# Kernel tuning notes

Hardware: AMD Instinct MI355X
Metric: run time of the kernel (lower is better)

The kernel has to match this reference:

```python
import jax, jax.numpy as jnp
import numpy as np

B = 8192
DIM = 1024
NI = 16
ALPHA = 0.5
BETA = 1.0


def setup_inputs() -> dict:
    key = jax.random.key(0)
    ks = jax.random.split(key, 12)
    d, n = DIM, NI
    din = d + d // n  # local expert input width = 1088
    s = 0.02  # small init scale to keep softplus in a sane range
    return {
        "y": jax.random.normal(ks[0], (B, d), jnp.float32),
        "M": jax.random.normal(ks[1], (B, d), jnp.float32),
        # global discriminator params ([in, out] layout)
        "gw0": jax.random.normal(ks[2], (d, d), jnp.float32) * s,
        "gb0": jnp.zeros((d,), jnp.float32),
        "gw1": jax.random.normal(ks[3], (d, d), jnp.float32) * s,
        "gb1": jnp.zeros((d,), jnp.float32),
        "l0w": jax.random.normal(ks[4], (2 * d, 128), jnp.float32) * s,
        "l0b": jnp.zeros((128,), jnp.float32),
        "l1w": jax.random.normal(ks[5], (128, 128), jnp.float32) * s,
        "l1b": jnp.zeros((128,), jnp.float32),
        "l2w": jax.random.normal(ks[6], (128, 1), jnp.float32) * s,
        "l2b": jnp.zeros((1,), jnp.float32),
        # local discriminator: n_interpretator stacked expert MLPs
        "lW1": jax.random.normal(ks[7], (n, din, 128), jnp.float32) * s,
        "lb1": jnp.zeros((n, 128), jnp.float32),
        "lW2": jax.random.normal(ks[8], (n, 128, 128), jnp.float32) * s,
        "lb2": jnp.zeros((n, 128), jnp.float32),
        "lW3": jax.random.normal(ks[9], (n, 128, 1), jnp.float32) * s,
        "lb3": jnp.zeros((n, 1), jnp.float32),
        "n_interpretator": NI,
    }


def reference(y, M, gw0, gb0, gw1, gb1, l0w, l0b, l1w, l1b, l2w, l2b,
              lW1, lb1, lW2, lb2, lW3, lb3, n_interpretator):
    n = n_interpretator
    Bsz, d = y.shape
    M3 = M.reshape(Bsz, d // n, n)                              # [B, d/n, n]
    Mp3 = jnp.concatenate([M3[1:], M3[:1]], axis=0)             # shuffled negatives
    y_exp = jnp.broadcast_to(y[:, :, None], (Bsz, d, n))        # [B, d, n]
    yM = jnp.concatenate([M3, y_exp], axis=1)                   # [B, d/n + d, n]
    yMp = jnp.concatenate([Mp3, y_exp], axis=1)

    def local_d(x):
        # batched over the n expert groups: grouped GEMMs instead of a loop
        h = jax.nn.relu(jnp.einsum('bdn,ndh->bnh', x, lW1) + lb1)   # [B, n, 128]
        h = jax.nn.relu(jnp.einsum('bnh,nhk->bnk', h, lW2) + lb2)   # [B, n, 128]
        s = jnp.einsum('bnh,nho->bno', h, lW3) + lb3                # [B, n, 1]
        return s[..., 0]                                            # [B, n]

    Ej_l = -jnp.mean(jax.nn.softplus(-local_d(yM)))
    Em_l = jnp.mean(jax.nn.softplus(local_d(yMp)))
    LOCAL = (Em_l - Ej_l) * BETA

    def global_d(yy, Mm):
        h = jax.nn.relu(Mm.reshape(Bsz, -1) @ gw0 + gb0) @ gw1 + gb1  # net(M)
        h = jnp.concatenate([yy, h], axis=1)                          # [B, 2d]
        h = jax.nn.relu(h @ l0w + l0b)
        h = jax.nn.relu(h @ l1w + l1b)
        return h @ l2w + l2b                                          # [B, 1]

    Ej_g = -jnp.mean(jax.nn.softplus(-global_d(y, M3)))
    Em_g = jnp.mean(jax.nn.softplus(global_d(y, Mp3)))
    GLOBAL = (Em_g - Ej_g) * ALPHA

    return LOCAL + GLOBAL
```

## Files before the change

kernel.cpp:

```cpp
#include <hip/hip_runtime.h>
#include <hip/hip_bf16.h>
#include <math.h>

#define B_ROWS 8192
#define NEXP 16

typedef __attribute__((ext_vector_type(8))) short short8;
typedef __attribute__((ext_vector_type(4))) float f32x4;

__device__ __forceinline__ float softplus_f(float x) {
    return fmaxf(x, 0.f) + log1pf(expf(-fabsf(x)));
}

__device__ __forceinline__ float bf2f(short u) {
    union { unsigned int i; float f; } c;
    c.i = ((unsigned int)(unsigned short)u) << 16;
    return c.f;
}

__device__ __forceinline__ short f2bf_s(float x) {
    __hip_bfloat16 h = __float2bfloat16(x);
    return *(short*)&h;
}

__device__ __forceinline__ void gll16(const void* g, void* l) {
    __builtin_amdgcn_global_load_lds(
        (const __attribute__((address_space(1))) void*)g,
        (__attribute__((address_space(3))) void*)l, 16, 0, 0);
}

#define FENCE() asm volatile("" ::: "memory")
#define VM3 asm volatile("s_waitcnt vmcnt(3)" ::: "memory")
#define VM0 asm volatile("s_waitcnt vmcnt(0)" ::: "memory")
#define BAR __builtin_amdgcn_s_barrier()

__device__ void cast_body(const float* in, __hip_bfloat16* out, int blk, int tid) {
    int i = blk * 256 + tid;
    float4 v = ((const float4*)in)[i];
    union { ushort4 u; __hip_bfloat16 h[4]; } p;
    p.h[0] = __float2bfloat16(v.x);
    p.h[1] = __float2bfloat16(v.y);
    p.h[2] = __float2bfloat16(v.z);
    p.h[3] = __float2bfloat16(v.w);
    ((ushort4*)out)[i] = p.u;
}

__global__ __launch_bounds__(256) void prep_all(
    const float* __restrict__ y, const float* __restrict__ M,
    const float* __restrict__ lW1, const float* __restrict__ gw0,
    const float* __restrict__ l0w, const float* __restrict__ gb1,
    const float* __restrict__ l0b, const float* __restrict__ lW2,
    const float* __restrict__ l1w, const float* __restrict__ gw1,
    __hip_bfloat16* __restrict__ yb, short* __restrict__ Mt2,
    __hip_bfloat16* __restrict__ W1yt, short* __restrict__ W1m2,
    __hip_bfloat16* __restrict__ W0p, __hip_bfloat16* __restrict__ l0wyt,
    float* __restrict__ bing, short* __restrict__ W2sb,
    short* __restrict__ L1ws, __hip_bfloat16* __restrict__ WgTb,
    double* __restrict__ acc, int* __restrict__ counter)
{
    __shared__ __align__(16) char smem[66048];
    const int b = blockIdx.x;
    const int tid = threadIdx.x;
    const int lane = tid & 63, w = tid >> 6;

    if (b < 8) {
        short* As = (short*)smem;
        short* Bs = (short*)(smem + 16384);
        const int bn = b * 128;
        const int wr = w >> 1, wc = w & 1;
        const int l15 = lane & 15, l4 = lane >> 4;

        f32x4 acc4[4][4] = {};
        for (int k0 = 0; k0 < 1024; k0 += 64) {
            {
                int c4 = (tid & 31) * 4;
                int kkr0 = tid >> 5;
                #pragma unroll
                for (int r = 0; r < 8; ++r) {
                    int kk = r * 8 + kkr0;
                    float4 v = *(const float4*)&l0w[(long)(1024 + k0 + kk) * 128 + c4];
                    int g = kk >> 3, sub = kk & 7;
                    #pragma unroll
                    for (int i = 0; i < 4; ++i) {
                        int row = c4 + i;
                        As[row * 64 + (g ^ (row & 7)) * 8 + sub] = f2bf_s(((const float*)&v)[i]);
                    }
                }
            }
            {
                int jr0 = tid >> 3;
                int g = tid & 7;
                #pragma unroll
                for (int s = 0; s < 4; ++s) {
                    int jrel = s * 32 + jr0;
                    const float* src = &gw1[(long)(bn + jrel) * 1024 + k0 + g * 8];
                    float4 v0 = *(const float4*)src;
                    float4 v1 = *(const float4*)(src + 4);
                    union { short8 v; short sh[8]; } o;
                    o.sh[0] = f2bf_s(v0.x); o.sh[1] = f2bf_s(v0.y);
                    o.sh[2] = f2bf_s(v0.z); o.sh[3] = f2bf_s(v0.w);
                    o.sh[4] = f2bf_s(v1.x); o.sh[5] = f2bf_s(v1.y);
                    o.sh[6] = f2bf_s(v1.z); o.sh[7] = f2bf_s(v1.w);
                    *(short8*)&Bs[jrel * 64 + (g ^ (jrel & 7)) * 8] = o.v;
                }
            }
            __syncthreads();
            #pragma unroll
            for (int st = 0; st < 2; ++st) {
                const int gr = (st * 4 + l4) ^ (l15 & 7);
                short8 a[4], bv[4];
                #pragma unroll
                for (int m = 0; m < 4; ++m)
                    a[m] = *(const short8*)&As[(wr * 64 + m * 16 + l15) * 64 + gr * 8];
                #pragma unroll
                for (int n = 0; n < 4; ++n)
                    bv[n] = *(const short8*)&Bs[(wc * 64 + n * 16 + l15) * 64 + gr * 8];
                #pragma unroll
                for (int m = 0; m < 4; ++m)
                    #pragma unroll
                    for (int n = 0; n < 4; ++n)
                        acc4[m][n] = __builtin_amdgcn_mfma_f32_16x16x32_bf16(a[m], bv[n], acc4[m][n], 0, 0, 0);
            }
            __syncthreads();
        }
        #pragma unroll
        for (int m = 0; m < 4; ++m) {
            int row = wr * 64 + m * 16 + l4 * 4;
            #pragma unroll
            for (int n = 0; n < 4; ++n) {
                int col = bn + wc * 64 + n * 16 + l15;
                #pragma unroll
                for (int r = 0; r < 4; ++r)
                    WgTb[(long)(row + r) * 1024 + col] = __float2bfloat16(acc4[m][n][r]);
            }
        }
        return;
    }

    if (b < 8200) { cast_body(y, yb, b - 8, tid); return; }

    if (b < 9224) {
        short* t = (short*)smem;
        const long r0 = (long)(b - 8200) * 8;
        #pragma unroll
        for (int i = 0; i < 8; ++i) {
            int idx = i * 1024 + tid * 4;
            float4 v = *(const float4*)&M[r0 * 1024 + idx];
            short4 s;
            s.x = f2bf_s(v.x); s.y = f2bf_s(v.y); s.z = f2bf_s(v.z); s.w = f2bf_s(v.w);
            *(short4*)&t[idx] = s;
        }
        __syncthreads();
        const int e = tid & 15, rr = (tid >> 4) & 7, hf = tid >> 7;
        #pragma unroll
        for (int c = 0; c < 4; ++c) {
            union { short8 v; short s[8]; } o;
            #pragma unroll
            for (int j = 0; j < 8; ++j)
                o.s[j] = t[rr * 1024 + (hf * 32 + c * 8 + j) * 16 + e];
            *(short8*)&Mt2[(long)(e >> 1) * (8192L * 128) + (r0 + rr) * 128
                           + (e & 1) * 64 + hf * 32 + c * 8] = o.v;
        }
        return;
    }

    float (*t)[129] = (float(*)[129])smem;

    if (b < 9736) {
        int l = b - 9224, bx = l & 15, by = l >> 4;
        int n0 = bx * 128, k0 = by * 32;
        long base = 64L * 128 + (long)bx * (1088L * 128);
        #pragma unroll
        for (int ll = 0; ll < 16; ++ll) {
            int idx = tid + ll * 256;
            int kk = idx >> 7, nn = idx & 127;
            t[kk][nn] = lW1[base + (long)(k0 + kk) * 128 + nn];
        }
        __syncthreads();
        int nn = tid >> 1, kb = (tid & 1) * 16;
        #pragma unroll
        for (int j = 0; j < 16; ++j)
            W1yt[(long)(n0 + nn) * 1024 + k0 + kb + j] = __float2bfloat16(t[kb + j][nn]);
        return;
    }

    if (b < 9768) {
        int l = b - 9736, bx = l & 15, by = l >> 4;
        int n0 = bx * 128, k0 = by * 32;
        long base = (long)bx * (1088L * 128);
        #pragma unroll
        for (int ll = 0; ll < 16; ++ll) {
            int idx = tid + ll * 256;
            int kk = idx >> 7, nn = idx & 127;
            if (kk < 32) t[kk][nn] = lW1[base + (long)(k0 + kk) * 128 + nn];
        }
        __syncthreads();
        int nn = tid >> 1, kb = (tid & 1) * 16;
        int half = bx & 1;
        #pragma unroll
        for (int j = 0; j < 16; ++j) {
            W1m2[(long)(n0 + nn) * 128 + half * 64 + k0 + kb + j] = f2bf_s(t[kb + j][nn]);
            W1m2[(long)(n0 + nn) * 128 + (1 - half) * 64 + k0 + kb + j] = 0;
        }
        return;
    }

    if (b < 10024) {
        int l = b - 9768, bx = l & 7, by = l >> 3;
        int n0 = bx * 128, k0 = by * 32;
        int e = k0 >> 6, dd0 = k0 & 63;
        #pragma unroll
        for (int ll = 0; ll < 16; ++ll) {
            int idx = tid + ll * 256;
            int kk = idx >> 7, nn = idx & 127;
            t[kk][nn] = gw0[(long)((dd0 + kk) * 16 + e) * 1024 + n0 + nn];
        }
        __syncthreads();
        int nn = tid >> 1, kb = (tid & 1) * 16;
        #pragma unroll
        for (int j = 0; j < 16; ++j)
            W0p[(long)(n0 + nn) * 1024 + k0 + kb + j] = __float2bfloat16(t[kb + j][nn]);
        return;
    }

    if (b < 10056) {
        int by = b - 10024;
        int k0 = by * 32;
        #pragma unroll
        for (int ll = 0; ll < 16; ++ll) {
            int idx = tid + ll * 256;
            int kk = idx >> 7, nn = idx & 127;
            t[kk][nn] = l0w[(long)(k0 + kk) * 128 + nn];
        }
        __syncthreads();
        int nn = tid >> 1, kb = (tid & 1) * 16;
        #pragma unroll
        for (int j = 0; j < 16; ++j)
            l0wyt[(long)nn * 1024 + k0 + kb + j] = __float2bfloat16(t[kb + j][nn]);
        return;
    }

    if (b == 10056) {
        if (tid < 128) {
            float s = l0b[tid];
            for (int o = 0; o < 1024; ++o)
                s = fmaf(gb1[o], l0w[(1024 + o) * 128 + tid], s);
            bing[tid] = s;
        }
        if (tid == 255) { acc[0] = 0.0; acc[1] = 0.0; *counter = 0; }
        return;
    }

    {
        int bb = b - 10057;
        const float* in = (bb < 16) ? lW2 + (long)bb * 16384 : l1w;
        short* out = (bb < 16) ? W2sb + (long)bb * 16384 : L1ws;
        #pragma unroll
        for (int l = 0; l < 64; ++l) {
            int idx = l * 256 + tid;
            t[idx >> 7][idx & 127] = in[idx];
        }
        __syncthreads();
        #pragma unroll
        for (int l = 0; l < 8; ++l) {
            int c = l * 256 + tid;
            int col = c >> 4, kc = c & 15;
            int kcs = kc ^ (col & 7);
            union { short8 v; short s[8]; } u;
            #pragma unroll
            for (int j = 0; j < 8; ++j)
                u.s[j] = f2bf_s(t[kc * 8 + j][col]);
            *(short8*)&out[col * 128 + kcs * 8] = u.v;
        }
    }
}

__global__ __launch_bounds__(512, 4) void gemm3s(
    const short* __restrict__ yb, const short* __restrict__ W1yt,
    __hip_bfloat16* __restrict__ Y1b,
    const short* __restrict__ Mt2, const short* __restrict__ W1m2,
    __hip_bfloat16* __restrict__ Mpb,
    const short* __restrict__ W0p, const float* __restrict__ gb0,
    __hip_bfloat16* __restrict__ H0b)
{
    __shared__ __align__(16) char smem[73728];
    const int tid = threadIdx.x;
    const int lane = tid & 63, w = tid >> 6;
    const int l15 = lane & 15, l4 = lane >> 4;
    const int wr = w >> 2, wc = w & 3;

    const int bid = blockIdx.x;
    const int xcd = bid & 7;
    const int idx = bid >> 3;

    int grp, bm, bn, K;
    const short* A; const short* Wt; __hip_bfloat16* C; int ldc;
    if (idx < 64) {
        grp = 0; const int c = idx >> 3, r = idx & 7;
        bm = (xcd * 8 + r) * 128; bn = c * 256;
        A = yb; Wt = W1yt + (long)bn * 1024; K = 1024; C = Y1b; ldc = 2048;
    } else if (idx < 96) {
        int j = idx - 64; const int c = j >> 3, r = j & 7;
        grp = 2; bm = (xcd * 8 + r) * 128; bn = c * 256;
        A = Mt2; Wt = W0p + (long)bn * 1024; K = 1024; C = H0b; ldc = 1024;
    } else {
        int j = idx - 96; const int c = j >> 3, r = j & 7;
        grp = 1; bm = (xcd * 8 + r) * 128; bn = c * 256;
        A = Mt2 + (long)c * (8192L * 128);
        Wt = W1m2 + (long)bn * 128; K = 128; C = Mpb; ldc = 2048;
    }
    const int nt = K >> 5;

    const int rowA = tid >> 2;
    const int sgA  = (tid & 3) ^ ((rowA >> 1) & 3);
    const int rowB0 = tid >> 2;
    const int sgB0  = (tid & 3) ^ ((rowB0 >> 1) & 3);
    const int rowB1 = (tid + 512) >> 2;
    const int sgB1  = (tid & 3) ^ ((rowB1 >> 1) & 3);

    auto STAGE = [&](int t, int sl) {
        char* base = smem + sl * 24576;
        const short* asrc;
        if (grp == 2) {
            const int g = t * 4 + sgA;
            asrc = A + (long)(g >> 4) * (8192L * 128)
                     + (long)(bm + rowA) * 128 + (g & 15) * 8;
        } else {
            asrc = A + (long)(bm + rowA) * K + t * 32 + sgA * 8;
        }
        gll16(asrc, base + w * 1024);
        gll16(Wt + (long)rowB0 * K + t * 32 + sgB0 * 8,
              base + 8192 + w * 1024);
        gll16(Wt + (long)rowB1 * K + t * 32 + sgB1 * 8,
              base + 16384 + w * 1024);
    };

    f32x4 acc[4][4] = {};
    const int xr = (l4 ^ ((l15 >> 1) & 3)) * 16;
    const int aOff = (wr * 64 + l15) * 64 + xr;
    const int bOff = 8192 + (wc * 64 + l15) * 64 + xr;

    auto PHASE = [&](int sl, int tn, int sl2, int mode) {
        const char* base = smem + sl * 24576;
        short8 a_[4], b_[4];
        #pragma unroll
        for (int m = 0; m < 4; ++m)
            a_[m] = *(const short8*)(base + aOff + m * 1024);
        #pragma unroll
        for (int n = 0; n < 4; ++n)
            b_[n] = *(const short8*)(base + bOff + n * 1024);
        if (mode == 0) { STAGE(tn, sl2); VM3; }
        else if (mode == 1) { VM0; }
        FENCE(); BAR; FENCE();
        __builtin_amdgcn_s_setprio(1);
        #pragma unroll
        for (int m = 0; m < 4; ++m)
            #pragma unroll
            for (int n = 0; n < 4; ++n)
                acc[m][n] = __builtin_amdgcn_mfma_f32_16x16x32_bf16(
                    a_[m], b_[n], acc[m][n], 0, 0, 0);
        __builtin_amdgcn_s_setprio(0);
        FENCE(); BAR; FENCE();
    };

    STAGE(0, 0);
    STAGE(1, 1);
    VM3; FENCE(); BAR; FENCE();

    int sl = 0, sl2 = 2;
    for (int t = 0; t < nt - 2; ++t) {
        PHASE(sl, t + 2, sl2, 0);
        sl = (sl == 2) ? 0 : sl + 1;
        sl2 = (sl2 == 2) ? 0 : sl2 + 1;
    }
    PHASE(sl, 0, 0, 1);
    sl = (sl == 2) ? 0 : sl + 1;
    PHASE(sl, 0, 0, 2);

    #pragma unroll
    for (int m = 0; m < 4; ++m) {
        const int row = bm + wr * 64 + m * 16 + l4 * 4;
        #pragma unroll
        for (int n = 0; n < 4; ++n) {
            const int col = bn + wc * 64 + n * 16 + l15;
            const float bv = (grp == 2) ? gb0[col] : 0.f;
            #pragma unroll
            for (int r = 0; r < 4; ++r) {
                float v = acc[m][n][r] + bv;
                if (grp == 2) v = fmaxf(v, 0.f);
                C[(long)(row + r) * ldc + col] = __float2bfloat16(v);
            }
        }
    }
}

__global__ __launch_bounds__(256) void tail_plus(
    const __hip_bfloat16* __restrict__ Yp, const __hip_bfloat16* __restrict__ Mq,
    const float* __restrict__ bin, const short* __restrict__ W2s,
    const float* __restrict__ b2, const float* __restrict__ w3,
    const float* __restrict__ b3, double* __restrict__ acc,
    const short* __restrict__ H0b, const short* __restrict__ WgTb,
    __hip_bfloat16* __restrict__ Tgb,
    const short* __restrict__ ybs, const short* __restrict__ l0ws,
    __hip_bfloat16* __restrict__ Tyb)
{
    __shared__ __align__(16) char smem[68096];
    const int bid = blockIdx.x;
    const int tid = threadIdx.x;
    const int lane = tid & 63;
    const int l15 = lane & 15, l4 = lane >> 4;

    if (bid >= 2048) {
        const int sel = bid - 2048;
        const short* Ain = (sel < 64) ? H0b : ybs;
        const short* Bin = (sel < 64) ? WgTb : l0ws;
        __hip_bfloat16* Co = (sel < 64) ? Tgb : Tyb;
        short* As = (short*)smem;
        short* Bs = (short*)(smem + 16384);
        const int w = tid >> 6;
        const int wr = w >> 1, wc = w & 1;
        const int bm = (sel & 63) * 128;
        const int srow = lane >> 3;
        const int gsrc = (lane & 7) ^ srow;

        f32x4 a4[4][4] = {};
        for (int k0 = 0; k0 < 1024; k0 += 64) {
            #pragma unroll
            for (int s = 0; s < 4; ++s) {
                const int rrel = s * 32 + w * 8 + srow;
                gll16(Ain + (long)(bm + rrel) * 1024 + k0 + gsrc * 8,
                      As + (s * 32 + w * 8) * 64);
                gll16(Bin + (long)rrel * 1024 + k0 + gsrc * 8,
                      Bs + (s * 32 + w * 8) * 64);
            }
            __syncthreads();
            #pragma unroll
            for (int st = 0; st < 2; ++st) {
                const int gr = (st * 4 + l4) ^ (l15 & 7);
                short8 a[4], b[4];
                #pragma unroll
                for (int m = 0; m < 4; ++m)
                    a[m] = *(const short8*)&As[(wr * 64 + m * 16 + l15) * 64 + gr * 8];
                #pragma unroll
                for (int n = 0; n < 4; ++n)
                    b[n] = *(const short8*)&Bs[(wc * 64 + n * 16 + l15) * 64 + gr * 8];
                #pragma unroll
                for (int m = 0; m < 4; ++m)
                    #pragma unroll
                    for (int n = 0; n < 4; ++n)
                        a4[m][n] = __builtin_amdgcn_mfma_f32_16x16x32_bf16(a[m], b[n], a4[m][n], 0, 0, 0);
            }
            __syncthreads();
        }
        #pragma unroll
        for (int m = 0; m < 4; ++m) {
            int row = bm + (w >> 1) * 64 + m * 16 + l4 * 4;
            #pragma unroll
            for (int n = 0; n < 4; ++n) {
                int col = (w & 1) * 64 + n * 16 + l15;
                #pragma unroll
                for (int r = 0; r < 4; ++r)
                    Co[(long)(row + r) * 128 + col] = __float2bfloat16(a4[m][n][r]);
            }
        }
        return;
    }

    const int wkid = (bid & 7) * 256 + (bid >> 3);
    const int e = wkid & 15;
    const int b0 = (wkid >> 4) * 64;
    const int cbase = e * 128;
    const int wid = tid >> 6;
    const int side = wid >> 1;
    const int wr = wid & 1;
    const int widthIn = 2048;

    short* h1 = (short*)smem;
    short* Bs = (short*)(smem + 32768);
    float* bins = (float*)(smem + 65536);
    float* b2s  = (float*)(smem + 66048);
    float* w3s  = (float*)(smem + 66560);
    float* red  = (float*)(smem + 67072);

    const short* W2e = W2s + (long)e * 16384;
    #pragma unroll
    for (int l = 0; l < 8; ++l) {
        int cb = (l * 4 + wid) * 64;
        gll16(W2e + (long)(cb + lane) * 8, &Bs[cb * 8]);
    }
    if (tid < 128) {
        bins[tid] = bin[cbase + tid];
        b2s[tid]  = b2[cbase + tid];
        w3s[tid]  = w3[cbase + tid];
    }
    __syncthreads();

    const short* Ys = (const short*)Yp;
    const short* Ms = (const short*)Mq;
    #pragma unroll
    for (int c = 0; c < 4; ++c) {
        int chunk = c * 256 + tid;
        int row = chunk >> 4, kc = chunk & 15;
        short8 yv = *(const short8*)&Ys[(long)(b0 + row) * widthIn + cbase + kc * 8];
        float yf[8];
        #pragma unroll
        for (int j = 0; j < 8; ++j) yf[j] = bf2f(yv[j]) + bins[kc * 8 + j];
        int dst = row * 128 + (kc ^ (row & 7)) * 8;
        #pragma unroll
        for (int s = 0; s < 2; ++s) {
            int rowm = (b0 + row + s) & (B_ROWS - 1);
            short8 mv = *(const short8*)&Ms[(long)rowm * widthIn + cbase + kc * 8];
            union { short8 v; short sh[8]; } o;
            #pragma unroll
            for (int j = 0; j < 8; ++j)
                o.sh[j] = f2bf_s(fmaxf(yf[j] + bf2f(mv[j]), 0.f));
            *(short8*)&h1[s * 8192 + dst] = o.v;
        }
    }
    __syncthreads();

    f32x4 accv[2][8] = {};
    #pragma unroll
    for (int st = 0; st < 4; ++st) {
        short8 a[2], b[8];
        #pragma unroll
        for (int m = 0; m < 2; ++m) {
            int row = wr * 32 + m * 16 + l15;
            int ch = (st * 4 + l4) ^ (row & 7);
            a[m] = *(const short8*)&h1[side * 8192 + row * 128 + ch * 8];
        }
        #pragma unroll
        for (int n = 0; n < 8; ++n) {
            int col = n * 16 + l15;
            int ch = (st * 4 + l4) ^ (col & 7);
            b[n] = *(const short8*)&Bs[col * 128 + ch * 8];
        }
        #pragma unroll
        for (int m = 0; m < 2; ++m)
            #pragma unroll
            for (int n = 0; n < 8; ++n)
                accv[m][n] = __builtin_amdgcn_mfma_f32_16x16x32_bf16(a[m], b[n], accv[m][n], 0, 0, 0);
    }

    float p[2][4] = {};
    #pragma unroll
    for (int m = 0; m < 2; ++m)
        #pragma unroll
        for (int n = 0; n < 8; ++n) {
            int colL = n * 16 + l15;
            float bb = b2s[colL], ww = w3s[colL];
            #pragma unroll
            for (int r = 0; r < 4; ++r) {
                float h2 = fmaxf(accv[m][n][r] + bb, 0.f);
                p[m][r] = fmaf(h2, ww, p[m][r]);
            }
        }
    #pragma unroll
    for (int m = 0; m < 2; ++m)
        #pragma unroll
        for (int r = 0; r < 4; ++r)
            #pragma unroll
            for (int off = 1; off < 16; off <<= 1)
                p[m][r] += __shfl_xor(p[m][r], off, 64);

    float mysum = 0.f;
    if (l15 == 0) {
        float bb = b3[e];
        #pragma unroll
        for (int m = 0; m < 2; ++m)
            #pragma unroll
            for (int r = 0; r < 4; ++r) {
                float s = p[m][r] + bb;
                mysum += softplus_f(side ? s : -s);
            }
    }
    red[tid] = mysum;
    __syncthreads();
    for (int s2 = 128; s2 > 0; s2 >>= 1) {
        if (tid < s2) red[tid] += red[tid + s2];
        __syncthreads();
    }
    if (tid == 0) atomicAdd(acc, (double)red[0]);
}

__global__ __launch_bounds__(256) void tail_mfma(
    const __hip_bfloat16* __restrict__ Yp, const __hip_bfloat16* __restrict__ Mq,
    const float* __restrict__ bin,
    const short* __restrict__ W2s,
    const float* __restrict__ b2, const float* __restrict__ w3,
    const float* __restrict__ b3,
    int widthIn, double* __restrict__ acc, int* __restrict__ counter,
    float* __restrict__ out)
{
    const int b0 = blockIdx.x * 64;
    const int e = blockIdx.y;
    const int cbase = e * 128;
    const int tid = threadIdx.x;
    const int lane = tid & 63;
    const int wid = tid >> 6;
    const int side = wid >> 1;
    const int wr = wid & 1;

    __shared__ __align__(16) short h1[2 * 64 * 128];
    __shared__ __align__(16) short Bs[128 * 128];
    __shared__ float bins[128], b2s[128], w3s[128];
    __shared__ float red[256];

    const short* W2e = W2s + (long)e * 16384;
    #pragma unroll
    for (int l = 0; l < 8; ++l) {
        int cb = (l * 4 + wid) * 64;
        gll16(W2e + (long)(cb + lane) * 8, &Bs[cb * 8]);
    }
    if (tid < 128) {
        bins[tid] = bin[cbase + tid];
        b2s[tid]  = b2[cbase + tid];
        w3s[tid]  = w3[cbase + tid];
    }
    __syncthreads();

    const short* Ys = (const short*)Yp;
    const short* Ms = (const short*)Mq;
    #pragma unroll
    for (int c = 0; c < 4; ++c) {
        int chunk = c * 256 + tid;
        int row = chunk >> 4, kc = chunk & 15;
        short8 yv = *(const short8*)&Ys[(long)(b0 + row) * widthIn + cbase + kc * 8];
        float yf[8];
        #pragma unroll
        for (int j = 0; j < 8; ++j) yf[j] = bf2f(yv[j]) + bins[kc * 8 + j];
        int dst = row * 128 + (kc ^ (row & 7)) * 8;
        #pragma unroll
        for (int s = 0; s < 2; ++s) {
            int rowm = (b0 + row + s) & (B_ROWS - 1);
            short8 mv = *(const short8*)&Ms[(long)rowm * widthIn + cbase + kc * 8];
            union { short8 v; short sh[8]; } o;
            #pragma unroll
            for (int j = 0; j < 8; ++j)
                o.sh[j] = f2bf_s(fmaxf(yf[j] + bf2f(mv[j]), 0.f));
            *(short8*)&h1[s * 8192 + dst] = o.v;
        }
    }
    __syncthreads();

    const int l15 = lane & 15, l4 = lane >> 4;
    f32x4 accv[2][8] = {};
    #pragma unroll
    for (int st = 0; st < 4; ++st) {
        short8 a[2], b[8];
        #pragma unroll
        for (int m = 0; m < 2; ++m) {
            int row = wr * 32 + m * 16 + l15;
            int ch = (st * 4 + l4) ^ (row & 7);
            a[m] = *(const short8*)&h1[side * 8192 + row * 128 + ch * 8];
        }
        #pragma unroll
        for (int n = 0; n < 8; ++n) {
            int col = n * 16 + l15;
            int ch = (st * 4 + l4) ^ (col & 7);
            b[n] = *(const short8*)&Bs[col * 128 + ch * 8];
        }
        #pragma unroll
        for (int m = 0; m < 2; ++m)
            #pragma unroll
            for (int n = 0; n < 8; ++n)
                accv[m][n] = __builtin_amdgcn_mfma_f32_16x16x32_bf16(a[m], b[n], accv[m][n], 0, 0, 0);
    }

    float p[2][4] = {};
    #pragma unroll
    for (int m = 0; m < 2; ++m)
        #pragma unroll
        for (int n = 0; n < 8; ++n) {
            int colL = n * 16 + l15;
            float bb = b2s[colL], ww = w3s[colL];
            #pragma unroll
            for (int r = 0; r < 4; ++r) {
                float h2 = fmaxf(accv[m][n][r] + bb, 0.f);
                p[m][r] = fmaf(h2, ww, p[m][r]);
            }
        }
    #pragma unroll
    for (int m = 0; m < 2; ++m)
        #pragma unroll
        for (int r = 0; r < 4; ++r)
            #pragma unroll
            for (int off = 1; off < 16; off <<= 1)
                p[m][r] += __shfl_xor(p[m][r], off, 64);

    float mysum = 0.f;
    if (l15 == 0) {
        float bb = b3[e];
        #pragma unroll
        for (int m = 0; m < 2; ++m)
            #pragma unroll
            for (int r = 0; r < 4; ++r) {
                float s = p[m][r] + bb;
                mysum += softplus_f(side ? s : -s);
            }
    }
    red[tid] = mysum;
    __syncthreads();
    for (int s2 = 128; s2 > 0; s2 >>= 1) {
        if (tid < s2) red[tid] += red[tid + s2];
        __syncthreads();
    }
    if (tid == 0) {
        atomicAdd(acc + 1, (double)red[0]);
        __threadfence();
        int old = atomicAdd(counter, 1);
        if (old == (int)(gridDim.x * gridDim.y) - 1) {
            double a0 = atomicAdd(acc + 0, 0.0);
            double a1 = atomicAdd(acc + 1, 0.0);
            out[0] = (float)(a0 / (8192.0 * 16.0) + 0.5 * a1 / 8192.0);
        }
    }
}

extern "C" void kernel_launch(void* const* d_in, const int* in_sizes, int n_in,
                              void* d_out, int out_size, void* d_ws, size_t ws_size,
                              hipStream_t stream)
{
    const float* y   = (const float*)d_in[0];
    const float* M   = (const float*)d_in[1];
    const float* gw0 = (const float*)d_in[2];
    const float* gb0 = (const float*)d_in[3];
    const float* gw1 = (const float*)d_in[4];
    const float* gb1 = (const float*)d_in[5];
    const float* l0w = (const float*)d_in[6];
    const float* l0b = (const float*)d_in[7];
    const float* l1w = (const float*)d_in[8];
    const float* l1b = (const float*)d_in[9];
    const float* l2w = (const float*)d_in[10];
    const float* l2b = (const float*)d_in[11];
    const float* lW1 = (const float*)d_in[12];
    const float* lb1 = (const float*)d_in[13];
    const float* lW2 = (const float*)d_in[14];
    const float* lb2 = (const float*)d_in[15];
    const float* lW3 = (const float*)d_in[16];
    const float* lb3 = (const float*)d_in[17];

    char* w = (char*)d_ws;
    double* acc = (double*)w;
    int* counter = (int*)(w + 16);
    float* bing = (float*)(w + 256);
    const size_t MB = 1u << 20;
    __hip_bfloat16* Y1b  = (__hip_bfloat16*)(w + 4096);
    __hip_bfloat16* Mpb  = (__hip_bfloat16*)(w + 4096 + 32 * MB);
    __hip_bfloat16* H0b  = (__hip_bfloat16*)(w + 4096 + 64 * MB);
    short*          Mt2  = (short*)(w + 4096 + 80 * MB);
    __hip_bfloat16* yb   = (__hip_bfloat16*)(w + 4096 + 96 * MB);
    __hip_bfloat16* W1yt = (__hip_bfloat16*)(w + 4096 + 112 * MB);
    __hip_bfloat16* W0p  = (__hip_bfloat16*)(w + 4096 + 118 * MB);
    __hip_bfloat16* l0wyt = (__hip_bfloat16*)(w + 4096 + 120 * MB);
    short* W2sb = (short*)(w + 4096 + 120 * MB + 512 * 1024);
    short* L1ws = (short*)(w + 4096 + 121 * MB);
    __hip_bfloat16* WgTb = (__hip_bfloat16*)(w + 4096 + 121 * MB + 512 * 1024);
    short* W1m2 = (short*)(w + 4096 + 122 * MB);
    __hip_bfloat16* Tyb = (__hip_bfloat16*)(w + 4096 + 123 * MB);
    __hip_bfloat16* Tgb = (__hip_bfloat16*)(w + 4096 + 125 * MB);

    dim3 blk(256);

    prep_all<<<dim3(10074), blk, 0, stream>>>(
        y, M, lW1, gw0, l0w, gb1, l0b, lW2, l1w, gw1,
        yb, Mt2, W1yt, W1m2, W0p, l0wyt, bing, W2sb, L1ws, WgTb,
        acc, counter);

    gemm3s<<<dim3(1280), dim3(512), 0, stream>>>(
        (const short*)yb, (const short*)W1yt, Y1b,
        Mt2, W1m2, Mpb,
        (const short*)W0p, gb0, H0b);

    tail_plus<<<dim3(2176), blk, 0, stream>>>(
        Y1b, Mpb, lb1, W2sb, lb2, lW3, lb3, acc,
        (const short*)H0b, (const short*)WgTb, Tgb,
        (const short*)yb, (const short*)l0wyt, Tyb);

    tail_mfma<<<dim3(128, 1), blk, 0, stream>>>(
        Tyb, Tgb, bing, L1ws, l1b, l2w, l2b, 128, acc, counter,
        (float*)d_out);
}
```

Baseline: 196.6 us.

## Split-K the weight-fold GEMM in prep and reduce partials inside gemm3s

The small weight-product GEMM in prep_all (8 blocks looping over all of K) becomes 64 blocks, each handling a 128-wide K slice and writing fp32 partials. Eight extra blocks appended to gemm3s sum the partials and cast them to bf16 WgTb. The y cast now does 8 float4 per thread over 1024 blocks instead of one per block, and the lW2/l1w transpose is done in two halves so shared memory halves. The aim is to stop the long serial GEMM blocks from becoming the tail of prep_all and to cut block count and LDS use. The cost is extra partial traffic, and the wgtp buffer aliases Tyb/Tgb, which are written only later in tail_plus.

```diff
diff --git a/kernel.cpp b/kernel.cpp
--- a/kernel.cpp
+++ b/kernel.cpp
@@ -33,17 +33,6 @@
 #define VM3 asm volatile("s_waitcnt vmcnt(3)" ::: "memory")
 #define VM0 asm volatile("s_waitcnt vmcnt(0)" ::: "memory")
 #define BAR __builtin_amdgcn_s_barrier()
-
-__device__ void cast_body(const float* in, __hip_bfloat16* out, int blk, int tid) {
-    int i = blk * 256 + tid;
-    float4 v = ((const float4*)in)[i];
-    union { ushort4 u; __hip_bfloat16 h[4]; } p;
-    p.h[0] = __float2bfloat16(v.x);
-    p.h[1] = __float2bfloat16(v.y);
-    p.h[2] = __float2bfloat16(v.z);
-    p.h[3] = __float2bfloat16(v.w);
-    ((ushort4*)out)[i] = p.u;
-}
 
 __global__ __launch_bounds__(256) void prep_all(
     const float* __restrict__ y, const float* __restrict__ M,
@@ -55,23 +44,25 @@
     __hip_bfloat16* __restrict__ W1yt, short* __restrict__ W1m2,
     __hip_bfloat16* __restrict__ W0p, __hip_bfloat16* __restrict__ l0wyt,
     float* __restrict__ bing, short* __restrict__ W2sb,
-    short* __restrict__ L1ws, __hip_bfloat16* __restrict__ WgTb,
+    short* __restrict__ L1ws, float* __restrict__ wgtp,
     double* __restrict__ acc, int* __restrict__ counter)
 {
-    __shared__ __align__(16) char smem[66048];
+    __shared__ __align__(16) char smem[33280];
     const int b = blockIdx.x;
     const int tid = threadIdx.x;
     const int lane = tid & 63, w = tid >> 6;
 
-    if (b < 8) {
+    if (b < 64) {
         short* As = (short*)smem;
         short* Bs = (short*)(smem + 16384);
-        const int bn = b * 128;
+        const int ct = b & 7, ks = b >> 3;
+        const int bn = ct * 128;
         const int wr = w >> 1, wc = w & 1;
         const int l15 = lane & 15, l4 = lane >> 4;
 
         f32x4 acc4[4][4] = {};
-        for (int k0 = 0; k0 < 1024; k0 += 64) {
+        for (int kq = 0; kq < 2; ++kq) {
+            const int k0 = ks * 128 + kq * 64;
             {
                 int c4 = (tid & 31) * 4;
                 int kkr0 = tid >> 5;
@@ -131,17 +122,31 @@
                 int col = bn + wc * 64 + n * 16 + l15;
                 #pragma unroll
                 for (int r = 0; r < 4; ++r)
-                    WgTb[(long)(row + r) * 1024 + col] = __float2bfloat16(acc4[m][n][r]);
-            }
-        }
-        return;
-    }
-
-    if (b < 8200) { cast_body(y, yb, b - 8, tid); return; }
-
-    if (b < 9224) {
+                    wgtp[((long)ks * 128 + row + r) * 1024 + col] = acc4[m][n][r];
+            }
+        }
+        return;
+    }
+
+    if (b < 1088) {
+        const long base = (long)(b - 64) * 2048;
+        #pragma unroll
+        for (int j = 0; j < 8; ++j) {
+            long i = base + j * 256 + tid;
+            float4 v = ((const float4*)y)[i];
+            union { ushort4 u; __hip_bfloat16 h[4]; } p;
+            p.h[0] = __float2bfloat16(v.x);
+            p.h[1] = __float2bfloat16(v.y);
+            p.h[2] = __float2bfloat16(v.z);
+            p.h[3] = __float2bfloat16(v.w);
+            ((ushort4*)yb)[i] = p.u;
+        }
+        return;
+    }
+
+    if (b < 2112) {
         short* t = (short*)smem;
-        const long r0 = (long)(b - 8200) * 8;
+        const long r0 = (long)(b - 1088) * 8;
         #pragma unroll
         for (int i = 0; i < 8; ++i) {
             int idx = i * 1024 + tid * 4;
@@ -166,8 +171,8 @@
 
     float (*t)[129] = (float(*)[129])smem;
 
-    if (b < 9736) {
-        int l = b - 9224, bx = l & 15, by = l >> 4;
+    if (b < 2624) {
+        int l = b - 2112, bx = l & 15, by = l >> 4;
         int n0 = bx * 128, k0 = by * 32;
         long base = 64L * 128 + (long)bx * (1088L * 128);
         #pragma unroll
@@ -184,8 +189,8 @@
         return;
     }
 
-    if (b < 9768) {
-        int l = b - 9736, bx = l & 15, by = l >> 4;
+    if (b < 2656) {
+        int l = b - 2624, bx = l & 15, by = l >> 4;
         int n0 = bx * 128, k0 = by * 32;
         long base = (long)bx * (1088L * 128);
         #pragma unroll
@@ -205,8 +210,8 @@
         return;
     }
 
-    if (b < 10024) {
-        int l = b - 9768, bx = l & 7, by = l >> 3;
+    if (b < 2912) {
+        int l = b - 2656, bx = l & 7, by = l >> 3;
         int n0 = bx * 128, k0 = by * 32;
         int e = k0 >> 6, dd0 = k0 & 63;
         #pragma unroll
@@ -223,8 +228,8 @@
         return;
     }
 
-    if (b < 10056) {
-        int by = b - 10024;
+    if (b < 2944) {
+        int by = b - 2912;
         int k0 = by * 32;
         #pragma unroll
         for (int ll = 0; ll < 16; ++ll) {
@@ -240,7 +245,7 @@
         return;
     }
 
-    if (b == 10056) {
+    if (b == 2944) {
         if (tid < 128) {
             float s = l0b[tid];
             for (int o = 0; o < 1024; ++o)
@@ -252,25 +257,31 @@
     }
 
     {
-        int bb = b - 10057;
+        int bb = b - 2945;
         const float* in = (bb < 16) ? lW2 + (long)bb * 16384 : l1w;
         short* out = (bb < 16) ? W2sb + (long)bb * 16384 : L1ws;
-        #pragma unroll
-        for (int l = 0; l < 64; ++l) {
-            int idx = l * 256 + tid;
-            t[idx >> 7][idx & 127] = in[idx];
-        }
-        __syncthreads();
-        #pragma unroll
-        for (int l = 0; l < 8; ++l) {
-            int c = l * 256 + tid;
-            int col = c >> 4, kc = c & 15;
-            int kcs = kc ^ (col & 7);
-            union { short8 v; short s[8]; } u;
-            #pragma unroll
-            for (int j = 0; j < 8; ++j)
-                u.s[j] = f2bf_s(t[kc * 8 + j][col]);
-            *(short8*)&out[col * 128 + kcs * 8] = u.v;
+        float (*t2)[65] = (float(*)[65])smem;
+        #pragma unroll
+        for (int h = 0; h < 2; ++h) {
+            if (h) __syncthreads();
+            #pragma unroll
+            for (int l = 0; l < 32; ++l) {
+                int idx = l * 256 + tid;
+                int kk = idx >> 6, cc = idx & 63;
+                t2[kk][cc] = in[(long)kk * 128 + h * 64 + cc];
+            }
+            __syncthreads();
+            #pragma unroll
+            for (int l = 0; l < 4; ++l) {
+                int c2 = l * 256 + tid;
+                int col = h * 64 + (c2 >> 4), kc = c2 & 15;
+                int kcs = kc ^ (col & 7);
+                union { short8 v; short s[8]; } u;
+                #pragma unroll
+                for (int j = 0; j < 8; ++j)
+                    u.s[j] = f2bf_s(t2[kc * 8 + j][col - h * 64]);
+                *(short8*)&out[col * 128 + kcs * 8] = u.v;
+            }
         }
     }
 }
@@ -281,7 +292,8 @@
     const short* __restrict__ Mt2, const short* __restrict__ W1m2,
     __hip_bfloat16* __restrict__ Mpb,
     const short* __restrict__ W0p, const float* __restrict__ gb0,
-    __hip_bfloat16* __restrict__ H0b)
+    __hip_bfloat16* __restrict__ H0b,
+    const float* __restrict__ wgtp, __hip_bfloat16* __restrict__ WgTb)
 {
     __shared__ __align__(16) char smem[73728];
     const int tid = threadIdx.x;
@@ -290,6 +302,31 @@
     const int wr = w >> 2, wc = w & 3;
 
     const int bid = blockIdx.x;
+
+    if (bid >= 1280) {
+        const int rb = bid - 1280;
+        #pragma unroll
+        for (int j = 0; j < 8; ++j) {
+            int i4 = tid + j * 512;
+            int flat = i4 * 4;
+            int row = flat >> 7, cc = flat & 127;
+            const long base = (long)row * 1024 + rb * 128 + cc;
+            f32x4 s = {};
+            #pragma unroll
+            for (int ks = 0; ks < 8; ++ks) {
+                f32x4 v = *(const f32x4*)&wgtp[(long)ks * 131072 + base];
+                s += v;
+            }
+            union { ushort4 u; __hip_bfloat16 h[4]; } o;
+            o.h[0] = __float2bfloat16(s[0]);
+            o.h[1] = __float2bfloat16(s[1]);
+            o.h[2] = __float2bfloat16(s[2]);
+            o.h[3] = __float2bfloat16(s[3]);
+            *(ushort4*)&WgTb[base] = o.u;
+        }
+        return;
+    }
+
     const int xcd = bid & 7;
     const int idx = bid >> 3;
 
@@ -759,18 +796,20 @@
     short* W1m2 = (short*)(w + 4096 + 122 * MB);
     __hip_bfloat16* Tyb = (__hip_bfloat16*)(w + 4096 + 123 * MB);
     __hip_bfloat16* Tgb = (__hip_bfloat16*)(w + 4096 + 125 * MB);
+    float* wgtp = (float*)(w + 4096 + 123 * MB);
 
     dim3 blk(256);
 
-    prep_all<<<dim3(10074), blk, 0, stream>>>(
+    prep_all<<<dim3(2962), blk, 0, stream>>>(
         y, M, lW1, gw0, l0w, gb1, l0b, lW2, l1w, gw1,
-        yb, Mt2, W1yt, W1m2, W0p, l0wyt, bing, W2sb, L1ws, WgTb,
+        yb, Mt2, W1yt, W1m2, W0p, l0wyt, bing, W2sb, L1ws, wgtp,
         acc, counter);
 
-    gemm3s<<<dim3(1280), dim3(512), 0, stream>>>(
+    gemm3s<<<dim3(1288), dim3(512), 0, stream>>>(
         (const short*)yb, (const short*)W1yt, Y1b,
         Mt2, W1m2, Mpb,
-        (const short*)W0p, gb0, H0b);
+        (const short*)W0p, gb0, H0b,
+        wgtp, WgTb);
 
     tail_plus<<<dim3(2176), blk, 0, stream>>>(
         Y1b, Mpb, lb1, W2sb, lb2, lW3, lb3, acc,
```

Result: no change. 198.6 us (+1.0%).
